# Optimization experiments

Measured on AMD Instinct MI355X. Metric: run time of the kernel, lower is better.

## Reference

```python
import jax, jax.numpy as jnp
import numpy as np

ALPHA = 1.0

def setup_inputs() -> dict:
    key = jax.random.key(0)
    k1, k2 = jax.random.split(key)
    x = jax.random.normal(k1, (65536, 256), dtype=jnp.float32)
    clusters = jax.random.normal(k2, (256, 256), dtype=jnp.float32)
    return {"x": x, "clusters": clusters}

def reference(x, clusters):
    # squared euclidean distance via the GEMM trick (same math as
    # sum((x[:,None,:] - clusters[None,:,:])**2, axis=2) without the (n,k,d) blowup)
    x2 = jnp.sum(x * x, axis=1, keepdims=True)            # [n,1]
    c2 = jnp.sum(clusters * clusters, axis=1)             # [k]
    dist2 = x2 + c2[None, :] - 2.0 * (x @ clusters.T)     # [n,k]
    q = 1.0 / (1.0 + dist2 / ALPHA)
    q = jnp.power(q, (ALPHA + 1.0) / 2.0)
    q = q / jnp.sum(q, axis=1, keepdims=True)             # row-normalize
    return q
```

## Files before the change

### kernel.cpp

```cpp
#include <hip/hip_runtime.h>


typedef _Float16 f16x8 __attribute__((ext_vector_type(8)));
typedef float    f32x4 __attribute__((ext_vector_type(4)));

#define DIM    256
#define NCLUST 256

__global__ __launch_bounds__(64) void pre_kernel(const float* __restrict__ clusters,
                                                 _Float16* __restrict__ bfrag,
                                                 float* __restrict__ c2p1) {
    int b = blockIdx.x;
    int l = threadIdx.x;
    if (b < 128) {
        int s   = b >> 4;
        int t   = b & 15;
        int col = t * 16 + (l & 15);
        int k0  = s * 32 + (l >> 4) * 8;
        const f32x4* p = reinterpret_cast<const f32x4*>(clusters + col * DIM + k0);
        f32x4 a = p[0];
        f32x4 c = p[1];
        f16x8 h;
        h[0] = (_Float16)(-2.0f * a[0]); h[1] = (_Float16)(-2.0f * a[1]);
        h[2] = (_Float16)(-2.0f * a[2]); h[3] = (_Float16)(-2.0f * a[3]);
        h[4] = (_Float16)(-2.0f * c[0]); h[5] = (_Float16)(-2.0f * c[1]);
        h[6] = (_Float16)(-2.0f * c[2]); h[7] = (_Float16)(-2.0f * c[3]);
        reinterpret_cast<f16x8*>(bfrag)[b * 64 + l] = h;
    } else {
        int j = b - 128;
        const f32x4* p = reinterpret_cast<const f32x4*>(clusters + j * DIM);
        f32x4 v = p[l];
        float s = v[0] * v[0] + v[1] * v[1] + v[2] * v[2] + v[3] * v[3];
#pragma unroll
        for (int m = 32; m >= 1; m >>= 1) s += __shfl_xor(s, m, 64);
        if (l == 0) c2p1[j] = 1.0f + s;
    }
}

__global__ __launch_bounds__(1024, 1) void cluster_kernel(const float* __restrict__ x,
                                                          const f32x4* __restrict__ bfrag,
                                                          const float* __restrict__ c2p1,
                                                          float* __restrict__ out) {
    __shared__ __align__(16) _Float16 Bs[65536];

    const int tid  = threadIdx.x;
    const int lane = tid & 63;
    const int wave = tid >> 6;
    const int cl   = lane & 15;
    const int g    = lane >> 4;
    const int tile = blockIdx.x * 16 + wave;

    f32x4 ld[16];
    {
        const float* xr = x + (size_t)(tile * 16 + cl) * DIM + g * 8;
#pragma unroll
        for (int s = 0; s < 8; ++s) {
            ld[2 * s]     = *reinterpret_cast<const f32x4*>(xr + s * 32);
            ld[2 * s + 1] = *reinterpret_cast<const f32x4*>(xr + s * 32 + 4);
        }
    }

    {
        f32x4* dst = reinterpret_cast<f32x4*>(Bs);
#pragma unroll
        for (int i = 0; i < 8; ++i) {
            int idx = i * 1024 + tid;
            dst[idx] = bfrag[idx];
        }
    }
    __syncthreads();

    f16x8 af[8];
    float x2p = 0.0f;
#pragma unroll
    for (int s = 0; s < 8; ++s) {
        f32x4 a = ld[2 * s], b = ld[2 * s + 1];
        x2p += a[0]*a[0] + a[1]*a[1] + a[2]*a[2] + a[3]*a[3]
             + b[0]*b[0] + b[1]*b[1] + b[2]*b[2] + b[3]*b[3];
        af[s][0] = (_Float16)a[0]; af[s][1] = (_Float16)a[1];
        af[s][2] = (_Float16)a[2]; af[s][3] = (_Float16)a[3];
        af[s][4] = (_Float16)b[0]; af[s][5] = (_Float16)b[1];
        af[s][6] = (_Float16)b[2]; af[s][7] = (_Float16)b[3];
    }
    float x2full = x2p + __shfl_xor(x2p, 16, 64);
    x2full += __shfl_xor(x2full, 32, 64);

    f32x4 acc[16];
#pragma unroll
    for (int t = 0; t < 16; ++t) {
        acc[t][0] = 0.f; acc[t][1] = 0.f; acc[t][2] = 0.f; acc[t][3] = 0.f;
    }
    const char* bsb = reinterpret_cast<const char*>(Bs) + lane * 16;
    __builtin_amdgcn_s_setprio(1);
#pragma unroll
    for (int s = 0; s < 8; ++s) {
#pragma unroll
        for (int t = 0; t < 16; ++t) {
            f16x8 bf = *reinterpret_cast<const f16x8*>(bsb + (s * 16 + t) * 1024);
            acc[t] = __builtin_amdgcn_mfma_f32_16x16x32_f16(af[s], bf, acc[t], 0, 0, 0);
        }
    }
    __builtin_amdgcn_s_setprio(0);

    float c2v[16];
#pragma unroll
    for (int t = 0; t < 16; ++t) c2v[t] = c2p1[t * 16 + cl];

    float x2j[4];
#pragma unroll
    for (int j = 0; j < 4; ++j) x2j[j] = __shfl(x2full, g * 4 + j, 64);

    float rsum[4] = {0.f, 0.f, 0.f, 0.f};
#pragma unroll
    for (int t = 0; t < 16; ++t) {
#pragma unroll
        for (int j = 0; j < 4; ++j) {
            float d = x2j[j] + c2v[t] + acc[t][j];
            float q = __builtin_amdgcn_rcpf(d);
            acc[t][j] = q;
            rsum[j] += q;
        }
    }
#pragma unroll
    for (int j = 0; j < 4; ++j) {
        float v = rsum[j];
        v += __shfl_xor(v, 1, 64); v += __shfl_xor(v, 2, 64);
        v += __shfl_xor(v, 4, 64); v += __shfl_xor(v, 8, 64);
        rsum[j] = __builtin_amdgcn_rcpf(v);
    }
    float* ob = out + (size_t)(tile * 16) * NCLUST;
#pragma unroll
    for (int t = 0; t < 16; ++t)
#pragma unroll
        for (int j = 0; j < 4; ++j)
            ob[(g * 4 + j) * NCLUST + t * 16 + cl] = acc[t][j] * rsum[j];
}

extern "C" void kernel_launch(void* const* d_in, const int* in_sizes, int n_in,
                              void* d_out, int out_size, void* d_ws, size_t ws_size,
                              hipStream_t stream) {
    const float* x        = (const float*)d_in[0];
    const float* clusters = (const float*)d_in[1];
    float* out = (float*)d_out;

    _Float16* bfrag = (_Float16*)d_ws;
    float*    c2p1  = (float*)((char*)d_ws + 128 * 64 * 16);

    pre_kernel<<<384, 64, 0, stream>>>(clusters, bfrag, c2p1);

    int nrows = in_sizes[0] / DIM;
    int grid  = nrows / (16 * 16);
    cluster_kernel<<<grid, 1024, 0, stream>>>(x, (const f32x4*)bfrag, c2p1, out);
}
```

Baseline: 37.53 us.

## Read B fragments directly from global/L2 with single-wave blocks instead of LDS staging

```diff
diff --git a/kernel.cpp b/kernel.cpp
--- a/kernel.cpp
+++ b/kernel.cpp
@@ -37,18 +37,14 @@
     }
 }
 
-__global__ __launch_bounds__(1024, 1) void cluster_kernel(const float* __restrict__ x,
-                                                          const f32x4* __restrict__ bfrag,
-                                                          const float* __restrict__ c2p1,
-                                                          float* __restrict__ out) {
-    __shared__ __align__(16) _Float16 Bs[65536];
-
-    const int tid  = threadIdx.x;
-    const int lane = tid & 63;
-    const int wave = tid >> 6;
+__global__ __launch_bounds__(64, 4) void cluster_kernel(const float* __restrict__ x,
+                                                        const f16x8* __restrict__ bfrag,
+                                                        const float* __restrict__ c2p1,
+                                                        float* __restrict__ out) {
+    const int lane = threadIdx.x;
     const int cl   = lane & 15;
     const int g    = lane >> 4;
-    const int tile = blockIdx.x * 16 + wave;
+    const int tile = blockIdx.x;
 
     f32x4 ld[16];
     {
@@ -59,16 +55,6 @@
             ld[2 * s + 1] = *reinterpret_cast<const f32x4*>(xr + s * 32 + 4);
         }
     }
-
-    {
-        f32x4* dst = reinterpret_cast<f32x4*>(Bs);
-#pragma unroll
-        for (int i = 0; i < 8; ++i) {
-            int idx = i * 1024 + tid;
-            dst[idx] = bfrag[idx];
-        }
-    }
-    __syncthreads();
 
     f16x8 af[8];
     float x2p = 0.0f;
@@ -90,17 +76,21 @@
     for (int t = 0; t < 16; ++t) {
         acc[t][0] = 0.f; acc[t][1] = 0.f; acc[t][2] = 0.f; acc[t][3] = 0.f;
     }
-    const char* bsb = reinterpret_cast<const char*>(Bs) + lane * 16;
-    __builtin_amdgcn_s_setprio(1);
+    const f16x8* bp = bfrag + lane;
 #pragma unroll
     for (int s = 0; s < 8; ++s) {
 #pragma unroll
-        for (int t = 0; t < 16; ++t) {
-            f16x8 bf = *reinterpret_cast<const f16x8*>(bsb + (s * 16 + t) * 1024);
-            acc[t] = __builtin_amdgcn_mfma_f32_16x16x32_f16(af[s], bf, acc[t], 0, 0, 0);
+        for (int tg = 0; tg < 4; ++tg) {
+            f16x8 bf[4];
+#pragma unroll
+            for (int u = 0; u < 4; ++u)
+                bf[u] = bp[(s * 16 + tg * 4 + u) * 64];
+#pragma unroll
+            for (int u = 0; u < 4; ++u)
+                acc[tg * 4 + u] = __builtin_amdgcn_mfma_f32_16x16x32_f16(
+                    af[s], bf[u], acc[tg * 4 + u], 0, 0, 0);
         }
     }
-    __builtin_amdgcn_s_setprio(0);
 
     float c2v[16];
 #pragma unroll
@@ -149,6 +139,6 @@
     pre_kernel<<<384, 64, 0, stream>>>(clusters, bfrag, c2p1);
 
     int nrows = in_sizes[0] / DIM;
-    int grid  = nrows / (16 * 16);
-    cluster_kernel<<<grid, 1024, 0, stream>>>(x, (const f32x4*)bfrag, c2p1, out);
+    int grid  = nrows / 16;
+    cluster_kernel<<<grid, 64, 0, stream>>>(x, (const f16x8*)bfrag, c2p1, out);
 }
```

Measured after the change: 42.86 us. +14.2%, slower.
